# Optimization experiments

Measured on AMD Instinct MI355X. Metric: run time of the kernel, lower is better.

Reference implementation:

```python
import jax, jax.numpy as jnp
import numpy as np

N_SEEDS = 2500
N_JOINTS = 24
D_FEAT = 131


def setup_inputs() -> dict:
    key = jax.random.key(0)
    k1, k2, k3, k4, k5 = jax.random.split(key, 5)
    B = 256
    seed_features = jax.random.normal(k1, (B, N_SEEDS, D_FEAT), dtype=jnp.float32)
    # Conv1d kernel_size=1 weights == matrices over the channel dim
    s1 = 1.0 / np.sqrt(N_SEEDS)
    s2 = 1.0 / np.sqrt(N_JOINTS)
    W1 = jax.random.uniform(k2, (N_JOINTS, N_SEEDS), jnp.float32, -s1, s1)
    b1 = jax.random.uniform(k3, (N_JOINTS,), jnp.float32, -s1, s1)
    W2 = jax.random.uniform(k4, (N_JOINTS, N_JOINTS), jnp.float32, -s2, s2)
    b2 = jax.random.uniform(k5, (N_JOINTS,), jnp.float32, -s2, s2)
    return {"seed_features": seed_features, "W1": W1, "b1": b1, "W2": W2, "b2": b2}


def reference(seed_features, W1, b1, W2, b2):
    # conv1d(k=1) over channels: [B,2500,131] -> [B,24,131]
    h = jax.nn.relu(jnp.einsum('oc,bcl->bol', W1, seed_features) + b1[None, :, None])
    query = jnp.einsum('oc,bcl->bol', W2, h) + b2[None, :, None]        # [B,24,131]
    scores = jnp.einsum('bjl,bnl->bjn', query, seed_features)            # [B,24,2500]
    attention = jax.nn.softmax(scores, axis=-1)
    output = jnp.einsum('bjn,bnl->bjl', attention, seed_features)        # [B,24,131]
    return output, attention
```

## Files before the change

### kernel.cpp

```cpp
#include <hip/hip_runtime.h>
#include <cstdint>
#include <cstddef>

#define NB 256
#define NS 2500
#define NJ 24
#define DF 131

#define QSEG 4
#define TSEG 640

#define KP 2528
#define XROWS 2528
#define LPq 136
#define CSP 66
#define OSTRIDE ((size_t)NB * NJ * DF)

using short8 = __attribute__((ext_vector_type(8))) short;
using f32x4  = __attribute__((ext_vector_type(4))) float;

#define F_XN   0ull
#define F_W1B  176029696ull
#define F_QBF  176191488ull
#define F_PO   178419712ull
#define F_MD   191297536ull
#define F_CS   191494144ull
#define F_P    191592448ull
#define WS_FULL 222656512ull

__device__ __forceinline__ unsigned short f2bf(float x) {
  union { float f; unsigned u; } v; v.f = x;
  unsigned r = v.u + 0x7fffu + ((v.u >> 16) & 1u);
  return (unsigned short)(r >> 16);
}
__device__ __forceinline__ float bf2f(unsigned us) {
  union { unsigned u; float f; } v; v.u = us << 16;
  return v.f;
}
__device__ __forceinline__ f32x4 mfma16(short8 a, short8 b, f32x4 c) {
  return __builtin_amdgcn_mfma_f32_16x16x32_bf16(a, b, c, 0, 0, 0);
}

__global__ __launch_bounds__(256) void kT2(const float* __restrict__ W1,
                                           unsigned short* __restrict__ W1b) {
  int dwi = blockIdx.x * 256 + threadIdx.x;
  if (dwi >= 32 * (KP / 2)) return;
  int row = dwi / (KP / 2);
  int kk = (dwi - row * (KP / 2)) * 2;
  unsigned lo = (row < NJ && kk     < NS) ? f2bf(W1[row * NS + kk])     : 0;
  unsigned hi = (row < NJ && kk + 1 < NS) ? f2bf(W1[row * NS + kk + 1]) : 0;
  ((unsigned*)W1b)[dwi] = lo | (hi << 16);
}

__global__ __launch_bounds__(256) void kPn(const float* __restrict__ sf,
                                           unsigned short* __restrict__ Xn) {
  int b = blockIdx.x / 20;
  int chunk = blockIdx.x - 20 * b;
  int c0 = chunk * 128;
  int w = threadIdx.x >> 6, lane = threadIdx.x & 63;
  const float* xb = sf + (size_t)b * (NS * DF);
  unsigned short* xnb = Xn + (size_t)b * ((size_t)XROWS * LPq);

#pragma unroll 4
  for (int i = 0; i < 32; ++i) {
    int r = w * 32 + i;
    int c = c0 + r;
    if (c >= XROWS) continue;
    bool vc = c < NS;
    const float* g = xb + (size_t)c * DF;
    float v0 = vc ? g[lane] : 0.f;
    float v1 = vc ? g[64 + lane] : 0.f;
    float v2 = (vc && lane < 3) ? g[128 + lane] : 0.f;
    unsigned short* d = xnb + (size_t)c * LPq;
    d[lane] = f2bf(v0);
    d[64 + lane] = f2bf(v1);
    if (lane < 8) d[128 + lane] = (lane < 3) ? f2bf(v2) : (unsigned short)0;
  }
}

__global__ __launch_bounds__(512) void kMM(const unsigned short* __restrict__ Xn,
                                           const unsigned short* __restrict__ A,
                                           int astride, int amax,
                                           float* __restrict__ Cp) {
  __shared__ unsigned short xs[2][144 * CSP];
  int b = blockIdx.x >> 2;
  int s = blockIdx.x & 3;
  int w = threadIdx.x >> 6, lane = threadIdx.x & 63;
  int lr = lane & 15, lg = lane >> 4;
  const unsigned* xb4 = (const unsigned*)(Xn + (size_t)b * ((size_t)XROWS * LPq));
  const unsigned short* Ab = A + (size_t)b * astride * KP;

  int nu = (w < 2) ? 3 : 2;
  f32x4 acc[3];
#pragma unroll
  for (int t = 0; t < 3; ++t) acc[t] = (f32x4){0.f, 0.f, 0.f, 0.f};

  int ch0 = s * 10;
  int q = lane & 3;
  unsigned pre[9];
#pragma unroll
  for (int k = 0; k < 8; ++k)
    pre[k] = xb4[(size_t)(ch0 * 64 + w * 8 + k) * (LPq / 2) + lane];
  pre[8] = 0;
  if (lane < 32)
    pre[8] = xb4[(size_t)(ch0 * 64 + w * 8 + (lane >> 2)) * (LPq / 2) + 64 + q];
#pragma unroll
  for (int k = 0; k < 8; ++k) {
    int r = w * 8 + k;
    xs[0][(2 * lane) * CSP + r]     = (unsigned short)(pre[k] & 0xffffu);
    xs[0][(2 * lane + 1) * CSP + r] = (unsigned short)(pre[k] >> 16);
  }
  if (lane < 32) {
    int r = w * 8 + (lane >> 2);
    int l0 = 128 + 2 * q;
    xs[0][l0 * CSP + r]       = (unsigned short)(pre[8] & 0xffffu);
    xs[0][(l0 + 1) * CSP + r] = (unsigned short)(pre[8] >> 16);
  }

  for (int i = 0; i < 10; ++i) {
    int ch = ch0 + i;
    int c0 = ch * 64;
    int CS = (ch < 39) ? 64 : 32;
    int cur = i & 1;
    __syncthreads();
    int CSn = 0;
    if (i + 1 < 10) {
      int c1 = c0 + 64;
      CSn = (ch + 1 < 39) ? 64 : 32;
#pragma unroll
      for (int k = 0; k < 8; ++k) {
        int r = w * 8 + k;
        pre[k] = (r < CSn) ? xb4[(size_t)(c1 + r) * (LPq / 2) + lane] : 0u;
      }
      pre[8] = 0;
      if (lane < 32) {
        int r = w * 8 + (lane >> 2);
        if (r < CSn)
          pre[8] = xb4[(size_t)(c1 + r) * (LPq / 2) + 64 + q];
      }
    }
    const unsigned* xc4 = (const unsigned*)xs[cur];
    int nks = CS >> 5;
    for (int ks = 0; ks < nks; ++ks) {
#pragma unroll
      for (int t = 0; t < 3; ++t) {
        if (t < nu) {
          int u = w + 8 * t;
          int m = u / 9, nt = u - 9 * m;
          int arow = m * 16 + lr; if (arow > amax) arow = amax;
          const unsigned short* ap = Ab + (size_t)arow * KP + c0 + ks * 32 + lg * 8;
          short8 av = *(const short8*)ap;
          int bb = (nt * 16 + lr) * (CSP / 2) + ks * 16 + lg * 4;
          unsigned b0 = xc4[bb], b1 = xc4[bb + 1], b2 = xc4[bb + 2], b3 = xc4[bb + 3];
          short8 bv;
          ((unsigned*)&bv)[0] = b0; ((unsigned*)&bv)[1] = b1;
          ((unsigned*)&bv)[2] = b2; ((unsigned*)&bv)[3] = b3;
          acc[t] = mfma16(av, bv, acc[t]);
        }
      }
    }
    if (i + 1 < 10) {
      unsigned short* xn = xs[cur ^ 1];
#pragma unroll
      for (int k = 0; k < 8; ++k) {
        int r = w * 8 + k;
        if (r < CSn) {
          xn[(2 * lane) * CSP + r]     = (unsigned short)(pre[k] & 0xffffu);
          xn[(2 * lane + 1) * CSP + r] = (unsigned short)(pre[k] >> 16);
        }
      }
      if (lane < 32) {
        int r = w * 8 + (lane >> 2);
        if (r < CSn) {
          int l0 = 128 + 2 * q;
          xn[l0 * CSP + r]       = (unsigned short)(pre[8] & 0xffffu);
          xn[(l0 + 1) * CSP + r] = (unsigned short)(pre[8] >> 16);
        }
      }
    }
  }
  float* Cb = Cp + (size_t)(s * NB + b) * (NJ * DF);
#pragma unroll
  for (int t = 0; t < 3; ++t) {
    if (t < nu) {
      int u = w + 8 * t;
      int m = u / 9, nt = u - 9 * m;
      int lcol = nt * 16 + lr;
      if (lcol < DF) {
#pragma unroll
        for (int r = 0; r < 4; ++r) {
          int j = m * 16 + lg * 4 + r;
          if (j < NJ) Cb[(size_t)j * DF + lcol] = acc[t][r];
        }
      }
    }
  }
}

__global__ __launch_bounds__(512) void kR4(const float* __restrict__ po,
                                           const float* __restrict__ csb,
                                           float* __restrict__ out) {
  int i = blockIdx.x * 512 + threadIdx.x;
  int bj = i / DF;
  const float* cs = csb + (size_t)bj * 4;
  out[i] = cs[0] * po[i] + cs[1] * po[OSTRIDE + i] +
           cs[2] * po[2 * OSTRIDE + i] + cs[3] * po[3 * OSTRIDE + i];
}

__global__ __launch_bounds__(512) void k1b(const float* __restrict__ po,
                                           const float* __restrict__ W2,
                                           const float* __restrict__ b1v,
                                           const float* __restrict__ b2v,
                                           unsigned short* __restrict__ qbf) {
  int flat = blockIdx.x * 512 + threadIdx.x;
  if (flat >= NB * LPq) return;
  int l = flat % LPq;
  int b = flat / LPq;
  unsigned short* qp = qbf + (size_t)b * (32 * LPq) + l;
  if (l >= DF) {
#pragma unroll
    for (int j = 0; j < 32; ++j) qp[j * LPq] = 0;
    return;
  }
  const float* p0 = po + (size_t)b * (NJ * DF) + l;
  float hv[NJ];
#pragma unroll
  for (int o = 0; o < NJ; ++o)
    hv[o] = fmaxf(b1v[o] + p0[o * DF] + p0[OSTRIDE + o * DF] +
                  p0[2 * OSTRIDE + o * DF] + p0[3 * OSTRIDE + o * DF], 0.f);
  float q[NJ];
  for (int o = 0; o < NJ; ++o) {
    float sv = b2v[o];
#pragma unroll
    for (int i = 0; i < NJ; ++i) sv = fmaf(W2[o * NJ + i], hv[i], sv);
    q[o] = sv;
  }
#pragma unroll
  for (int j = 0; j < NJ; ++j) qp[j * LPq] = f2bf(q[j]);
#pragma unroll
  for (int j = NJ; j < 32; ++j) qp[j * LPq] = 0;
}

__global__ __launch_bounds__(512) void k2m(const unsigned short* __restrict__ Xn,
                                           const unsigned short* __restrict__ qbf,
                                           unsigned short* __restrict__ P,
                                           float* __restrict__ md) {
  __shared__ float wm[8][24];
  __shared__ float wd[8][24];
  int b = blockIdx.x >> 2, seg = blockIdx.x & 3;
  int w = threadIdx.x >> 6, lane = threadIdx.x & 63;
  int lr = lane & 15, lg = lane >> 4;
  const short8 z8 = {0, 0, 0, 0, 0, 0, 0, 0};

  const unsigned short* qb = qbf + (size_t)b * (32 * LPq);
  short8 aq0[5], aq1[5];
#pragma unroll
  for (int ks = 0; ks < 4; ++ks) {
    aq0[ks] = *(const short8*)(qb + (size_t)lr * LPq + ks * 32 + lg * 8);
    aq1[ks] = *(const short8*)(qb + (size_t)(16 + lr) * LPq + ks * 32 + lg * 8);
  }
  aq0[4] = (lg == 0) ? *(const short8*)(qb + (size_t)lr * LPq + 128) : z8;
  aq1[4] = (lg == 0) ? *(const short8*)(qb + (size_t)(16 + lr) * LPq + 128) : z8;

  const unsigned short* xb = Xn + (size_t)b * ((size_t)XROWS * LPq);
  int ntl = (seg < 3) ? 40 : 37;

  f32x4 s0[5], s1[5];
  float m8[8];
#pragma unroll
  for (int r = 0; r < 8; ++r) m8[r] = -1e30f;

#pragma unroll
  for (int i = 0; i < 5; ++i) {
    s0[i] = (f32x4){0.f, 0.f, 0.f, 0.f};
    s1[i] = (f32x4){0.f, 0.f, 0.f, 0.f};
    int ti = w + 8 * i;
    if (ti < ntl) {
      int n = (seg * 40 + ti) * 16 + lr;
      const unsigned short* bp = xb + (size_t)n * LPq + lg * 8;
      short8 bx[5];
#pragma unroll
      for (int ks = 0; ks < 4; ++ks) bx[ks] = *(const short8*)(bp + ks * 32);
      bx[4] = (lg == 0) ? *(const short8*)(xb + (size_t)n * LPq + 128) : z8;
      f32x4 a0 = {0.f, 0.f, 0.f, 0.f}, a1 = {0.f, 0.f, 0.f, 0.f};
#pragma unroll
      for (int ks = 0; ks < 5; ++ks) {
        a0 = mfma16(aq0[ks], bx[ks], a0);
        a1 = mfma16(aq1[ks], bx[ks], a1);
      }
      s0[i] = a0; s1[i] = a1;
#pragma unroll
      for (int r = 0; r < 4; ++r) {
        m8[r]     = fmaxf(m8[r],     a0[r]);
        m8[4 + r] = fmaxf(m8[4 + r], a1[r]);
      }
    }
  }
#pragma unroll
  for (int r = 0; r < 8; ++r)
#pragma unroll
    for (int off = 1; off < 16; off <<= 1)
      m8[r] = fmaxf(m8[r], __shfl_xor(m8[r], off));
  if (lr == 0) {
#pragma unroll
    for (int r = 0; r < 4; ++r) {
      wm[w][lg * 4 + r] = m8[r];
      if (lg < 2) wm[w][16 + lg * 4 + r] = m8[4 + r];
    }
  }
  __syncthreads();
  float mseg[8];
#pragma unroll
  for (int r = 0; r < 4; ++r) {
    float m0 = wm[0][lg * 4 + r];
#pragma unroll
    for (int wv = 1; wv < 8; ++wv) m0 = fmaxf(m0, wm[wv][lg * 4 + r]);
    mseg[r] = m0;
    int j1 = 16 + (lg & 1) * 4 + r;
    float m1 = wm[0][j1];
#pragma unroll
    for (int wv = 1; wv < 8; ++wv) m1 = fmaxf(m1, wm[wv][j1]);
    mseg[4 + r] = m1;
  }
  float d8[8];
#pragma unroll
  for (int r = 0; r < 8; ++r) d8[r] = 0.f;
#pragma unroll
  for (int i = 0; i < 5; ++i) {
    int ti = w + 8 * i;
    if (ti < ntl) {
      int n = (seg * 40 + ti) * 16 + lr;
      bool valid = n < NS;
#pragma unroll
      for (int r = 0; r < 4; ++r) {
        float p0 = __expf(s0[i][r] - mseg[r]);
        float p1 = __expf(s1[i][r] - mseg[4 + r]);
        if (valid) {
          P[((size_t)b * NJ + lg * 4 + r) * KP + n] = f2bf(p0);
          d8[r] += p0;
          if (lg < 2) {
            P[((size_t)b * NJ + 16 + lg * 4 + r) * KP + n] = f2bf(p1);
            d8[4 + r] += p1;
          }
        }
      }
    }
  }
#pragma unroll
  for (int r = 0; r < 8; ++r)
#pragma unroll
    for (int off = 1; off < 16; off <<= 1)
      d8[r] += __shfl_xor(d8[r], off);
  if (lr == 0) {
#pragma unroll
    for (int r = 0; r < 4; ++r) {
      wd[w][lg * 4 + r] = d8[r];
      if (lg < 2) wd[w][16 + lg * 4 + r] = d8[4 + r];
    }
  }
  __syncthreads();
  if (threadIdx.x < NJ) {
    int j = threadIdx.x;
    float m = wm[0][j], d = 0.f;
#pragma unroll
    for (int wv = 1; wv < 8; ++wv) m = fmaxf(m, wm[wv][j]);
#pragma unroll
    for (int wv = 0; wv < 8; ++wv) d += wd[wv][j];
    float* mp = md + ((size_t)b * QSEG + seg) * 48;
    mp[j] = m;
    mp[24 + j] = d;
  }
}

__global__ __launch_bounds__(256) void kW(unsigned short* __restrict__ P,
                                          const float* __restrict__ md,
                                          float* __restrict__ attn,
                                          float* __restrict__ csb) {
  int bj = blockIdx.x;
  int b = bj / NJ, j = bj - b * NJ;
  const float* mp = md + (size_t)b * (QSEG * 48);
  float ms[QSEG];
  float m = -1e30f;
#pragma unroll
  for (int s = 0; s < QSEG; ++s) { ms[s] = mp[s * 48 + j]; m = fmaxf(m, ms[s]); }
  float d = 0.f;
#pragma unroll
  for (int s = 0; s < QSEG; ++s) d += mp[s * 48 + 24 + j] * __expf(ms[s] - m);
  float rinv = 1.f / d;
  float cs[QSEG];
#pragma unroll
  for (int s = 0; s < QSEG; ++s) cs[s] = __expf(ms[s] - m) * rinv;
  if (threadIdx.x < QSEG) {
    float v = cs[0];
    if (threadIdx.x == 1) v = cs[1];
    if (threadIdx.x == 2) v = cs[2];
    if (threadIdx.x == 3) v = cs[3];
    csb[(size_t)bj * QSEG + threadIdx.x] = v;
  }

  unsigned* prow = (unsigned*)(P + (size_t)bj * KP);
  float2* arow = (float2*)(attn + (size_t)bj * NS);
  for (int i = threadIdx.x; i < NS / 2; i += 256) {
    unsigned pk = prow[i];
    int n0 = 2 * i;
    float p0 = bf2f(pk & 0xffffu) * cs[n0 / TSEG];
    float p1 = bf2f(pk >> 16) * cs[(n0 + 1) / TSEG];
    arow[i] = make_float2(p0, p1);
  }
  if (threadIdx.x < (KP - NS) / 2) prow[NS / 2 + threadIdx.x] = 0;
}

#define KSEG 8
#define CSEG 313
#define SEGN 625
#define TN 64
#define LDP 132
#define WS_W1T 0u
#define WS_QTF 60000u
#define WS_MDF (WS_QTF + 804864u)
#define WS_PHF (WS_MDF + (unsigned)(NB * QSEG * 48))
#define SEGSTRIDE ((size_t)NB * NJ * DF)

__global__ __launch_bounds__(256) void kT_f(const float* __restrict__ W1,
                                            float* __restrict__ W1t) {
  int i = blockIdx.x * 256 + threadIdx.x;
  if (i >= NJ * NS) return;
  int o = i / NS, c = i - o * NS;
  W1t[c * NJ + o] = W1[i];
}

__global__ __launch_bounds__(192) void kH_f(const float* __restrict__ sf,
                                            const float* __restrict__ W1t,
                                            float* __restrict__ ph) {
  int b = blockIdx.x >> 3;
  int s = blockIdx.x & 7;
  int l = threadIdx.x;
  int c0 = s * CSEG;
  int cnt = NS - c0; if (cnt > CSEG) cnt = CSEG;
  const float* xp = sf + (size_t)b * (NS * DF) + (size_t)c0 * DF;
  const float* wp = W1t + (size_t)c0 * NJ;
  float acc[NJ];
#pragma unroll
  for (int o = 0; o < NJ; ++o) acc[o] = 0.f;
  if (l < DF) {
#pragma unroll 2
    for (int c = 0; c < cnt; ++c) {
      float xv = xp[(size_t)c * DF + l];
#pragma unroll
      for (int o = 0; o < NJ; ++o) acc[o] = fmaf(wp[c * NJ + o], xv, acc[o]);
    }
    float* pp = ph + (size_t)(s * NB + b) * (NJ * DF) + l;
#pragma unroll
    for (int o = 0; o < NJ; ++o) pp[o * DF] = acc[o];
  }
}

__global__ __launch_bounds__(512) void k1b_f(const float* __restrict__ ph,
                                             const float* __restrict__ W2,
                                             const float* __restrict__ b1v,
                                             const float* __restrict__ b2v,
                                             float* __restrict__ q_t) {
  int flat = blockIdx.x * 512 + threadIdx.x;
  if (flat >= NB * DF) return;
  int l = flat % DF;
  int b = flat / DF;
  const float* p0 = ph + (size_t)(b * NJ) * DF + l;
  float hv[NJ];
#pragma unroll
  for (int o = 0; o < NJ; ++o) hv[o] = b1v[o];
  for (int s = 0; s < KSEG; ++s) {
#pragma unroll
    for (int o = 0; o < NJ; ++o) hv[o] += p0[s * SEGSTRIDE + o * DF];
  }
#pragma unroll
  for (int o = 0; o < NJ; ++o) hv[o] = fmaxf(hv[o], 0.f);
  float q[NJ];
  for (int o = 0; o < NJ; ++o) {
    float sv = b2v[o];
#pragma unroll
    for (int i = 0; i < NJ; ++i) sv = fmaf(W2[o * NJ + i], hv[i], sv);
    q[o] = sv;
  }
  float4* qp = (float4*)(q_t + (size_t)flat * NJ);
#pragma unroll
  for (int v = 0; v < 6; ++v)
    qp[v] = make_float4(q[4 * v], q[4 * v + 1], q[4 * v + 2], q[4 * v + 3]);
}

__global__ __launch_bounds__(256) void k2_f(const float* __restrict__ sf,
                                            const float* __restrict__ q_t,
                                            float* __restrict__ raw,
                                            float* __restrict__ md) {
  __shared__ __align__(16) float xs[TN * LDP];
  int b = blockIdx.x >> 2;
  int s = blockIdx.x & 3;
  int tid = threadIdx.x;
  int wid = tid >> 6, lane = tid & 63;
  int jq = __builtin_amdgcn_readfirstlane(wid);

  const float* sft = sf + (size_t)b * (NS * DF) + (size_t)(s * SEGN) * DF;
  const float* qb = q_t + (size_t)b * (DF * NJ) + jq * 6;
  float* rawb = raw + (size_t)b * (NJ * NS) + (size_t)(s * SEGN);

  float m6[6], d6[6];
#pragma unroll
  for (int i = 0; i < 6; ++i) { m6[i] = -1e30f; d6[i] = 0.f; }

  const int NT = (SEGN + TN - 1) / TN;
  for (int t = 0; t < NT; ++t) {
    int n0 = t * TN;
    int nmax = SEGN - n0; if (nmax > TN) nmax = TN;
    __syncthreads();
#pragma unroll
    for (int rr = 0; rr < 16; ++rr) {
      int r = wid * 16 + rr;
      if (r < nmax) {
        const float* g = sft + (size_t)(n0 + r) * DF;
        float* d = xs + r * LDP;
        d[lane] = g[lane];
        d[64 + lane] = g[64 + lane];
        if (lane < 3) d[128 + lane] = g[128 + lane];
      }
    }
    __syncthreads();
    if (lane < nmax) {
      const float* xrow = xs + lane * LDP;
      float sa[6];
#pragma unroll
      for (int i = 0; i < 6; ++i) sa[i] = 0.f;
      for (int l4 = 0; l4 < 32; ++l4) {
        float4 xv = *(const float4*)(xrow + 4 * l4);
        const float* q4 = qb + (4 * l4) * NJ;
#pragma unroll
        for (int i = 0; i < 6; ++i) sa[i] = fmaf(q4[i], xv.x, sa[i]);
#pragma unroll
        for (int i = 0; i < 6; ++i) sa[i] = fmaf(q4[NJ + i], xv.y, sa[i]);
#pragma unroll
        for (int i = 0; i < 6; ++i) sa[i] = fmaf(q4[2 * NJ + i], xv.z, sa[i]);
#pragma unroll
        for (int i = 0; i < 6; ++i) sa[i] = fmaf(q4[3 * NJ + i], xv.w, sa[i]);
      }
#pragma unroll
      for (int l = 128; l < DF; ++l) {
        float xv = xrow[l];
#pragma unroll
        for (int i = 0; i < 6; ++i) sa[i] = fmaf(qb[l * NJ + i], xv, sa[i]);
      }
      int nr = n0 + lane;
#pragma unroll
      for (int i = 0; i < 6; ++i) {
        rawb[(size_t)(jq * 6 + i) * NS + nr] = sa[i];
        float mn = fmaxf(m6[i], sa[i]);
        d6[i] = d6[i] * __expf(m6[i] - mn) + __expf(sa[i] - mn);
        m6[i] = mn;
      }
    }
  }
#pragma unroll
  for (int i = 0; i < 6; ++i) {
    float m = m6[i], d = d6[i];
    for (int off = 32; off > 0; off >>= 1) {
      float mo = __shfl_xor(m, off);
      float dd = __shfl_xor(d, off);
      float nm = fmaxf(m, mo);
      d = d * __expf(m - nm) + dd * __expf(mo - nm);
      m = nm;
    }
    m6[i] = m; d6[i] = d;
  }
  if (lane == 0) {
    float* mp = md + ((size_t)b * QSEG + s) * 48;
#pragma unroll
    for (int i = 0; i < 6; ++i) {
      mp[jq * 6 + i] = m6[i];
      mp[24 + jq * 6 + i] = d6[i];
    }
  }
}

__global__ __launch_bounds__(256) void k3_f(float* __restrict__ attn,
                                            const float* __restrict__ md) {
  int bj = blockIdx.x;
  int b = bj / NJ;
  int j = bj - b * NJ;
  const float* mp = md + (size_t)b * (QSEG * 48);
  float m = -1e30f, d = 0.f;
#pragma unroll
  for (int s = 0; s < QSEG; ++s) {
    float ms = mp[s * 48 + j], ds = mp[s * 48 + 24 + j];
    float nm = fmaxf(m, ms);
    d = d * __expf(m - nm) + ds * __expf(ms - nm);
    m = nm;
  }
  float r = 1.f / d;
  float* p = attn + (size_t)bj * NS;
  for (int n = threadIdx.x; n < NS; n += 256)
    p[n] = __expf(p[n] - m) * r;
}

__global__ __launch_bounds__(192) void k4_f(const float* __restrict__ sf,
                                            const float* __restrict__ attn,
                                            float* __restrict__ po) {
  int b = blockIdx.x >> 3;
  int s = blockIdx.x & 7;
  int l = threadIdx.x;
  int n0 = s * CSEG;
  int cnt = NS - n0; if (cnt > CSEG) cnt = CSEG;
  const float* xp = sf + (size_t)b * (NS * DF) + (size_t)n0 * DF;
  const float* ap = attn + (size_t)b * (NJ * NS) + n0;
  float acc[NJ];
#pragma unroll
  for (int o = 0; o < NJ; ++o) acc[o] = 0.f;
  if (l < DF) {
#pragma unroll 2
    for (int n = 0; n < cnt; ++n) {
      float xv = xp[(size_t)n * DF + l];
#pragma unroll
      for (int o = 0; o < NJ; ++o) acc[o] = fmaf(ap[(size_t)o * NS + n], xv, acc[o]);
    }
    float* pp = po + (size_t)(s * NB + b) * (NJ * DF) + l;
#pragma unroll
    for (int o = 0; o < NJ; ++o) pp[o * DF] = acc[o];
  }
}

__global__ __launch_bounds__(512) void k5_f(const float* __restrict__ po,
                                            float* __restrict__ out) {
  int i = blockIdx.x * 512 + threadIdx.x;
  float v = 0.f;
#pragma unroll
  for (int s = 0; s < KSEG; ++s) v += po[s * SEGSTRIDE + i];
  out[i] = v;
}

extern "C" void kernel_launch(void* const* d_in, const int* in_sizes, int n_in,
                              void* d_out, int out_size, void* d_ws, size_t ws_size,
                              hipStream_t stream) {
  const float* sf = (const float*)d_in[0];
  const float* W1 = (const float*)d_in[1];
  const float* b1 = (const float*)d_in[2];
  const float* W2 = (const float*)d_in[3];
  const float* b2 = (const float*)d_in[4];
  float* out = (float*)d_out;
  float* attn = out + (size_t)NB * NJ * DF;

  if (ws_size >= WS_FULL) {
    unsigned short* Xn  = (unsigned short*)((char*)d_ws + F_XN);
    unsigned short* W1b = (unsigned short*)((char*)d_ws + F_W1B);
    unsigned short* qbf = (unsigned short*)((char*)d_ws + F_QBF);
    float* po   = (float*)((char*)d_ws + F_PO);
    float* md   = (float*)((char*)d_ws + F_MD);
    float* csb  = (float*)((char*)d_ws + F_CS);
    unsigned short* P   = (unsigned short*)((char*)d_ws + F_P);

    kT2<<<158, 256, 0, stream>>>(W1, W1b);
    kPn<<<NB * 20, 256, 0, stream>>>(sf, Xn);
    kMM<<<NB * 4, 512, 0, stream>>>(Xn, W1b, 0, 31, po);
    k1b<<<68, 512, 0, stream>>>(po, W2, b1, b2, qbf);
    k2m<<<NB * QSEG, 512, 0, stream>>>(Xn, qbf, P, md);
    kW <<<NB * NJ, 256, 0, stream>>>(P, md, attn, csb);
    kMM<<<NB * 4, 512, 0, stream>>>(Xn, P, NJ, 23, po);
    kR4<<<1572, 512, 0, stream>>>(po, csb, out);
  } else {
    float* ws = (float*)d_ws;
    float* W1t = ws + WS_W1T;
    float* q_t = ws + WS_QTF;
    float* md  = ws + WS_MDF;
    float* ph  = ws + WS_PHF;
    kT_f <<<235, 256, 0, stream>>>(W1, W1t);
    kH_f <<<NB * KSEG, 192, 0, stream>>>(sf, W1t, ph);
    k1b_f<<<66, 512, 0, stream>>>(ph, W2, b1, b2, q_t);
    k2_f <<<NB * QSEG, 256, 0, stream>>>(sf, q_t, attn, md);
    k3_f <<<NB * NJ, 256, 0, stream>>>(attn, md);
    k4_f <<<NB * KSEG, 192, 0, stream>>>(sf, attn, ph);
    k5_f <<<1572, 512, 0, stream>>>(ph, out);
  }
}
```

Baseline: 319.0 us.

## Fuse attention-times-features matmul into the scores/softmax kernel via LDS staging

Measured after the change: 364.1 us. +14.1%, slower.

```diff
diff --git a/kernel.cpp b/kernel.cpp
--- a/kernel.cpp
+++ b/kernel.cpp
@@ -14,6 +14,7 @@
 #define XROWS 2528
 #define LPq 136
 #define CSP 66
+#define PST 648
 #define OSTRIDE ((size_t)NB * NJ * DF)
 
 using short8 = __attribute__((ext_vector_type(8))) short;
@@ -241,12 +242,15 @@
   for (int j = NJ; j < 32; ++j) qp[j * LPq] = 0;
 }
 
-__global__ __launch_bounds__(512) void k2m(const unsigned short* __restrict__ Xn,
+__global__ __launch_bounds__(512) void kFA(const unsigned short* __restrict__ Xn,
                                            const unsigned short* __restrict__ qbf,
                                            unsigned short* __restrict__ P,
-                                           float* __restrict__ md) {
+                                           float* __restrict__ md,
+                                           float* __restrict__ Cp) {
   __shared__ float wm[8][24];
   __shared__ float wd[8][24];
+  __shared__ __align__(16) unsigned short pls[24 * PST];
+  __shared__ unsigned short xs[144 * CSP];
   int b = blockIdx.x >> 2, seg = blockIdx.x & 3;
   int w = threadIdx.x >> 6, lane = threadIdx.x & 63;
   int lr = lane & 15, lg = lane >> 4;
@@ -263,13 +267,13 @@
   aq1[4] = (lg == 0) ? *(const short8*)(qb + (size_t)(16 + lr) * LPq + 128) : z8;
 
   const unsigned short* xb = Xn + (size_t)b * ((size_t)XROWS * LPq);
+  const unsigned* xb4 = (const unsigned*)xb;
   int ntl = (seg < 3) ? 40 : 37;
 
   f32x4 s0[5], s1[5];
   float m8[8];
 #pragma unroll
   for (int r = 0; r < 8; ++r) m8[r] = -1e30f;
-
 #pragma unroll
   for (int i = 0; i < 5; ++i) {
     s0[i] = (f32x4){0.f, 0.f, 0.f, 0.f};
@@ -328,20 +332,25 @@
 #pragma unroll
   for (int i = 0; i < 5; ++i) {
     int ti = w + 8 * i;
-    if (ti < ntl) {
-      int n = (seg * 40 + ti) * 16 + lr;
-      bool valid = n < NS;
-#pragma unroll
-      for (int r = 0; r < 4; ++r) {
-        float p0 = __expf(s0[i][r] - mseg[r]);
-        float p1 = __expf(s1[i][r] - mseg[4 + r]);
+    int nlb = ti * 16 + lr;
+    int n = (seg * 40 + ti) * 16 + lr;
+    bool valid = (ti < ntl) && (n < NS);
+#pragma unroll
+    for (int r = 0; r < 4; ++r) {
+      float p0 = __expf(s0[i][r] - mseg[r]);
+      float p1 = __expf(s1[i][r] - mseg[4 + r]);
+      unsigned short pb0 = valid ? f2bf(p0) : (unsigned short)0;
+      pls[(lg * 4 + r) * PST + nlb] = pb0;
+      if (valid) {
+        P[((size_t)b * NJ + lg * 4 + r) * KP + n] = pb0;
+        d8[r] += p0;
+      }
+      if (lg < 2) {
+        unsigned short pb1 = valid ? f2bf(p1) : (unsigned short)0;
+        pls[(16 + lg * 4 + r) * PST + nlb] = pb1;
         if (valid) {
-          P[((size_t)b * NJ + lg * 4 + r) * KP + n] = f2bf(p0);
-          d8[r] += p0;
-          if (lg < 2) {
-            P[((size_t)b * NJ + 16 + lg * 4 + r) * KP + n] = f2bf(p1);
-            d8[4 + r] += p1;
-          }
+          P[((size_t)b * NJ + 16 + lg * 4 + r) * KP + n] = pb1;
+          d8[4 + r] += p1;
         }
       }
     }
@@ -369,6 +378,94 @@
     float* mp = md + ((size_t)b * QSEG + seg) * 48;
     mp[j] = m;
     mp[24 + j] = d;
+  }
+
+  int nu = (w < 2) ? 3 : 2;
+  f32x4 acc[3];
+#pragma unroll
+  for (int t = 0; t < 3; ++t) acc[t] = (f32x4){0.f, 0.f, 0.f, 0.f};
+  int ch0 = seg * 10;
+  int q = lane & 3;
+  unsigned pre[9];
+#pragma unroll
+  for (int k = 0; k < 8; ++k)
+    pre[k] = xb4[(size_t)(ch0 * 64 + w * 8 + k) * (LPq / 2) + lane];
+  pre[8] = 0;
+  if (lane < 32)
+    pre[8] = xb4[(size_t)(ch0 * 64 + w * 8 + (lane >> 2)) * (LPq / 2) + 64 + q];
+
+  for (int cl = 0; cl < 10; ++cl) {
+    int ch = ch0 + cl;
+    int CS = (ch < 39) ? 64 : 32;
+    __syncthreads();
+#pragma unroll
+    for (int k = 0; k < 8; ++k) {
+      int r = w * 8 + k;
+      if (r < CS) {
+        xs[(2 * lane) * CSP + r]     = (unsigned short)(pre[k] & 0xffffu);
+        xs[(2 * lane + 1) * CSP + r] = (unsigned short)(pre[k] >> 16);
+      }
+    }
+    if (lane < 32) {
+      int r = w * 8 + (lane >> 2);
+      if (r < CS) {
+        int l0 = 128 + 2 * q;
+        xs[l0 * CSP + r]       = (unsigned short)(pre[8] & 0xffffu);
+        xs[(l0 + 1) * CSP + r] = (unsigned short)(pre[8] >> 16);
+      }
+    }
+    __syncthreads();
+    if (cl + 1 < 10) {
+      int c1 = (ch + 1) * 64;
+      int CSn = (ch + 1 < 39) ? 64 : 32;
+#pragma unroll
+      for (int k = 0; k < 8; ++k) {
+        int r = w * 8 + k;
+        pre[k] = (r < CSn) ? xb4[(size_t)(c1 + r) * (LPq / 2) + lane] : 0u;
+      }
+      pre[8] = 0;
+      if (lane < 32) {
+        int r = w * 8 + (lane >> 2);
+        if (r < CSn)
+          pre[8] = xb4[(size_t)(c1 + r) * (LPq / 2) + 64 + q];
+      }
+    }
+    const unsigned* xc4 = (const unsigned*)xs;
+    int nks = CS >> 5;
+    for (int ks = 0; ks < nks; ++ks) {
+#pragma unroll
+      for (int t = 0; t < 3; ++t) {
+        if (t < nu) {
+          int u = w + 8 * t;
+          int m = u / 9, nt = u - 9 * m;
+          int arow = m * 16 + lr; if (arow > 23) arow = 23;
+          const unsigned short* ap = pls + (size_t)arow * PST + cl * 64 + ks * 32 + lg * 8;
+          short8 av = *(const short8*)ap;
+          int bb = (nt * 16 + lr) * (CSP / 2) + ks * 16 + lg * 4;
+          unsigned b0 = xc4[bb], b1 = xc4[bb + 1], b2 = xc4[bb + 2], b3 = xc4[bb + 3];
+          short8 bv;
+          ((unsigned*)&bv)[0] = b0; ((unsigned*)&bv)[1] = b1;
+          ((unsigned*)&bv)[2] = b2; ((unsigned*)&bv)[3] = b3;
+          acc[t] = mfma16(av, bv, acc[t]);
+        }
+      }
+    }
+  }
+  float* Cb = Cp + (size_t)(seg * NB + b) * (NJ * DF);
+#pragma unroll
+  for (int t = 0; t < 3; ++t) {
+    if (t < nu) {
+      int u = w + 8 * t;
+      int m = u / 9, nt = u - 9 * m;
+      int lcol = nt * 16 + lr;
+      if (lcol < DF) {
+#pragma unroll
+        for (int r = 0; r < 4; ++r) {
+          int j = m * 16 + lg * 4 + r;
+          if (j < NJ) Cb[(size_t)j * DF + lcol] = acc[t][r];
+        }
+      }
+    }
   }
 }
 
@@ -397,7 +494,6 @@
     if (threadIdx.x == 3) v = cs[3];
     csb[(size_t)bj * QSEG + threadIdx.x] = v;
   }
-
   unsigned* prow = (unsigned*)(P + (size_t)bj * KP);
   float2* arow = (float2*)(attn + (size_t)bj * NS);
   for (int i = threadIdx.x; i < NS / 2; i += 256) {
@@ -407,7 +503,6 @@
     float p1 = bf2f(pk >> 16) * cs[(n0 + 1) / TSEG];
     arow[i] = make_float2(p0, p1);
   }
-  if (threadIdx.x < (KP - NS) / 2) prow[NS / 2 + threadIdx.x] = 0;
 }
 
 #define KSEG 8
@@ -657,9 +752,8 @@
     kPn<<<NB * 20, 256, 0, stream>>>(sf, Xn);
     kMM<<<NB * 4, 512, 0, stream>>>(Xn, W1b, 0, 31, po);
     k1b<<<68, 512, 0, stream>>>(po, W2, b1, b2, qbf);
-    k2m<<<NB * QSEG, 512, 0, stream>>>(Xn, qbf, P, md);
+    kFA<<<NB * 4, 512, 0, stream>>>(Xn, qbf, P, md, po);
     kW <<<NB * NJ, 256, 0, stream>>>(P, md, attn, csb);
-    kMM<<<NB * 4, 512, 0, stream>>>(Xn, P, NJ, 23, po);
     kR4<<<1572, 512, 0, stream>>>(po, csb, out);
   } else {
     float* ws = (float*)d_ws;
```
